# Kernel optimization log

Hardware: AMD Instinct MI355X
Metric: run time of the kernel (lower is better)

The kernel has to match this reference:

```python
import jax, jax.numpy as jnp
import numpy as np

N_NODES = 100000

def gcn_conv(x, W, b, src, dst, n):
    # PyG GCNConv with add_self_loops=True, symmetric normalization.
    # Transform first (reduces feature dim before irregular aggregation).
    h = x @ W  # [N, out]
    # degree with self loops: in-degree over dst plus 1 per node
    deg = jax.ops.segment_sum(jnp.ones_like(dst, dtype=h.dtype), dst, num_segments=n) + 1.0
    dinv = jax.lax.rsqrt(deg)  # deg >= 1 due to self loops
    norm = dinv[src] * dinv[dst]  # [E]
    # message = norm * h[src], aggregated at dst; self-loop term = dinv_i^2 * h_i
    agg = jax.ops.segment_sum(h[src] * norm[:, None], dst, num_segments=n)
    agg = agg + h * (dinv * dinv)[:, None]
    return agg + b

def setup_inputs() -> dict:
    key = jax.random.key(0)
    k1, k2, k3, k4, k5 = jax.random.split(key, 5)
    F_in, H, E_dim = 128, 64, 64
    node_features = jax.random.normal(k1, (N_NODES, F_in), dtype=jnp.float32)
    edge_index = jax.random.randint(k2, (2, 1600000), 0, N_NODES, dtype=jnp.int64)
    s = 1.0 / np.sqrt(F_in)
    W1 = jax.random.uniform(k3, (F_in, H), jnp.float32, -s, s)
    b1 = jnp.zeros((H,), jnp.float32)
    s2 = 1.0 / np.sqrt(H)
    W2 = jax.random.uniform(k4, (H, H), jnp.float32, -s2, s2)
    b2 = jnp.zeros((H,), jnp.float32)
    Wl = jax.random.uniform(k5, (H, E_dim), jnp.float32, -s2, s2)
    bl = jnp.zeros((E_dim,), jnp.float32)
    return {"node_features": node_features, "edge_index": edge_index,
            "W1": W1, "b1": b1, "W2": W2, "b2": b2, "Wl": Wl, "bl": bl}

def reference(node_features, edge_index, W1, b1, W2, b2, Wl, bl):
    src, dst = edge_index[0], edge_index[1]
    n = node_features.shape[0]
    x = node_features.astype(jnp.float32)
    x = jax.nn.relu(gcn_conv(x, W1, b1, src, dst, n))
    # dropout: train=False -> identity
    x = jax.nn.relu(gcn_conv(x, W2, b2, src, dst, n))
    x = x @ Wl + bl
    return jax.nn.sigmoid(x).T  # [embed_size, N]
```

## Files before the change

### kernel.cpp

```cpp
#include <hip/hip_runtime.h>
#include <hip/hip_bf16.h>


#define FEAT 64
#define FIN 128
#define PAD 64
#define CAP 4608
#define EPB 4096
#define MAXNB 512

typedef __attribute__((ext_vector_type(8))) short  short8;
typedef __attribute__((ext_vector_type(4))) float  f32x4;

__device__ __forceinline__ unsigned short f2bf(float f) {
    union { float f; unsigned u; } x; x.f = f;
    unsigned r = x.u + 0x7FFF + ((x.u >> 16) & 1);
    return (unsigned short)(r >> 16);
}
__device__ __forceinline__ float bflo(unsigned u) {
    union { unsigned v; float f; } x; x.v = u << 16; return x.f;
}
__device__ __forceinline__ float bfhi(unsigned u) {
    union { unsigned v; float f; } x; x.v = u & 0xFFFF0000u; return x.f;
}

__global__ void wtrans_kernel(const float* __restrict__ W1, const float* __restrict__ W2,
                              unsigned short* __restrict__ Wt1, unsigned short* __restrict__ Wt2) {
    int t = blockIdx.x * 256 + threadIdx.x;
    if (t < FIN * 64) {
        int k = t >> 6, n = t & 63;
        Wt1[n * FIN + k] = f2bf(W1[t]);
    } else if (t < FIN * 64 + 64 * 64) {
        int u = t - FIN * 64;
        int k = u >> 6, n = u & 63;
        Wt2[n * 64 + k] = f2bf(W2[u]);
    }
}

__global__ __launch_bounds__(256) void bin_kernel(const int* __restrict__ ei,
                                                  int* __restrict__ bcnt,
                                                  int* __restrict__ bbuf,
                                                  int E, int nb) {
    __shared__ int hist[MAXNB];
    __shared__ int base[MAXNB];
    __shared__ int cur[MAXNB];
    for (int t = threadIdx.x; t < nb; t += 256) { hist[t] = 0; cur[t] = 0; }
    __syncthreads();
    int e0 = blockIdx.x * EPB;
    int sreg[16], dreg[16];
#pragma unroll
    for (int k = 0; k < 16; ++k) {
        int idx = e0 + k * 256 + threadIdx.x;
        if (idx < E) {
            sreg[k] = ei[idx];
            dreg[k] = ei[E + idx];
            atomicAdd(&hist[dreg[k] >> 8], 1);
        } else {
            dreg[k] = -1;
        }
    }
    __syncthreads();
    for (int t = threadIdx.x; t < nb; t += 256) {
        int h = hist[t];
        base[t] = (h > 0) ? atomicAdd(&bcnt[t * 16], h) : 0;
    }
    __syncthreads();
#pragma unroll
    for (int k = 0; k < 16; ++k) {
        if (dreg[k] >= 0) {
            int b = dreg[k] >> 8;
            int p = base[b] + atomicAdd(&cur[b], 1);
            if (p < CAP)
                bbuf[(size_t)b * CAP + p] = sreg[k] | ((dreg[k] & 255) << 20);
        }
    }
}

__global__ __launch_bounds__(256) void ell_from_bins_kernel(const int* __restrict__ bbuf,
                                                            const int* __restrict__ bcnt,
                                                            int* __restrict__ col,
                                                            int* __restrict__ cnt,
                                                            float* __restrict__ dinv,
                                                            unsigned int* __restrict__ gz,
                                                            int N) {
    __shared__ int lcnt[256];
    int b = blockIdx.x;
    int d0 = b << 8;
    lcnt[threadIdx.x] = 0;
    if (b == 0 && threadIdx.x < 32)
        gz[(size_t)N * 32 + threadIdx.x] = 0u;
    __syncthreads();
    int ne = bcnt[b * 16];
    if (ne > CAP) ne = CAP;
    const int* eb = bbuf + (size_t)b * CAP;
    for (int i = threadIdx.x; i < ne; i += 256) {
        int w = eb[i];
        int s = w & 0xFFFFF;
        int dl = w >> 20;
        int slot = atomicAdd(&lcnt[dl], 1);
        if (slot < PAD) col[(size_t)(d0 + dl) * PAD + slot] = s;
    }
    __syncthreads();
    int d = d0 + threadIdx.x;
    if (d < N) {
        int c = lcnt[threadIdx.x];
        if (c > PAD) c = PAD;
        int c8 = (c + 7) & ~7;
        for (int k = c; k < c8; ++k) col[(size_t)d * PAD + k] = N;
        cnt[d] = c;
        dinv[d] = rsqrtf((float)c + 1.0f);
    }
}

template<int K>
__global__ __launch_bounds__(256) void gemm_mfma_kernel(const float* __restrict__ x,
                                                        const unsigned short* __restrict__ Wt,
                                                        const float* __restrict__ dinv,
                                                        unsigned short* __restrict__ g, int N) {
    const int lane = threadIdx.x & 63;
    const int wave = threadIdx.x >> 6;
    const int m = lane & 15, quad = lane >> 4;
    const int r0 = blockIdx.x * 64 + wave * 16;
    const int arow = r0 + m;
    const bool aok = arow < N;
    f32x4 acc[4] = {f32x4{0,0,0,0}, f32x4{0,0,0,0}, f32x4{0,0,0,0}, f32x4{0,0,0,0}};
    union { short8 s; unsigned short u[8]; } a;
#pragma unroll
    for (int s = 0; s < K / 32; ++s) {
        if (aok) {
            const float* xp = x + (size_t)arow * K + s * 32 + quad * 8;
            float4 a0 = *(const float4*)xp;
            float4 a1 = *(const float4*)(xp + 4);
            a.u[0] = f2bf(a0.x); a.u[1] = f2bf(a0.y);
            a.u[2] = f2bf(a0.z); a.u[3] = f2bf(a0.w);
            a.u[4] = f2bf(a1.x); a.u[5] = f2bf(a1.y);
            a.u[6] = f2bf(a1.z); a.u[7] = f2bf(a1.w);
        } else {
#pragma unroll
            for (int k = 0; k < 8; ++k) a.u[k] = 0;
        }
#pragma unroll
        for (int t = 0; t < 4; ++t) {
            const unsigned short* bp = Wt + (size_t)(t * 16 + m) * K + s * 32 + quad * 8;
            short8 bf = *(const short8*)bp;
            acc[t] = __builtin_amdgcn_mfma_f32_16x16x32_bf16(a.s, bf, acc[t], 0, 0, 0);
        }
    }
    const int rbase = r0 + quad * 4;
#pragma unroll
    for (int i = 0; i < 4; ++i) {
        int r = rbase + i;
        if (r < N) {
            float di = dinv[r];
#pragma unroll
            for (int t = 0; t < 4; ++t)
                g[(size_t)r * 64 + t * 16 + m] = f2bf(di * acc[t][i]);
        }
    }
}

__global__ __launch_bounds__(256) void agg_relu_kernel(const unsigned short* __restrict__ g,
                                                       const int* __restrict__ cnt,
                                                       const int* __restrict__ col,
                                                       const float* __restrict__ dinv,
                                                       const float* __restrict__ b,
                                                       float* __restrict__ xout, int N) {
    int node = blockIdx.x * 4 + (threadIdx.x >> 6);
    if (node >= N) return;
    int lane = threadIdx.x & 63;
    int rg = lane >> 3, fc = lane & 7;
    int c = cnt[node];
    if (c > PAD) c = PAD;
    int c8 = (c + 7) & ~7;
    const int* cl = col + (size_t)node * PAD;
    float acc[8] = {0.f, 0.f, 0.f, 0.f, 0.f, 0.f, 0.f, 0.f};
#pragma unroll 2
    for (int j = 0; j < c8; j += 8) {
        int s = cl[j + rg];
        uint4 w = *(const uint4*)(g + (size_t)s * 64 + fc * 8);
        acc[0] += bflo(w.x); acc[1] += bfhi(w.x);
        acc[2] += bflo(w.y); acc[3] += bfhi(w.y);
        acc[4] += bflo(w.z); acc[5] += bfhi(w.z);
        acc[6] += bflo(w.w); acc[7] += bfhi(w.w);
    }
#pragma unroll
    for (int mk = 8; mk <= 32; mk <<= 1)
#pragma unroll
        for (int k = 0; k < 8; ++k)
            acc[k] += __shfl_xor(acc[k], mk, 64);
    if (rg == 0) {
        uint4 w = *(const uint4*)(g + (size_t)node * 64 + fc * 8);
        acc[0] += bflo(w.x); acc[1] += bfhi(w.x);
        acc[2] += bflo(w.y); acc[3] += bfhi(w.y);
        acc[4] += bflo(w.z); acc[5] += bfhi(w.z);
        acc[6] += bflo(w.w); acc[7] += bfhi(w.w);
        float di = dinv[node];
        float4 b0 = *(const float4*)&b[fc * 8];
        float4 b1 = *(const float4*)&b[fc * 8 + 4];
        float4 o0 = make_float4(fmaxf(di * acc[0] + b0.x, 0.f),
                                fmaxf(di * acc[1] + b0.y, 0.f),
                                fmaxf(di * acc[2] + b0.z, 0.f),
                                fmaxf(di * acc[3] + b0.w, 0.f));
        float4 o1 = make_float4(fmaxf(di * acc[4] + b1.x, 0.f),
                                fmaxf(di * acc[5] + b1.y, 0.f),
                                fmaxf(di * acc[6] + b1.z, 0.f),
                                fmaxf(di * acc[7] + b1.w, 0.f));
        *(float4*)&xout[(size_t)node * 64 + fc * 8]     = o0;
        *(float4*)&xout[(size_t)node * 64 + fc * 8 + 4] = o1;
    }
}

__global__ __launch_bounds__(256) void final_kernel(const float* __restrict__ x2,
                                                    const float* __restrict__ Wl,
                                                    const float* __restrict__ bl,
                                                    float* __restrict__ out, int N) {
    __shared__ float xs[64 * 68];
    __shared__ float ws[64 * 64];
    __shared__ float bls[64];
    const int tid = threadIdx.x;
    const int r0 = blockIdx.x * 64;
    for (int t = tid * 4; t < 64 * 64; t += 1024)
        *(float4*)&ws[t] = *(const float4*)&Wl[t];
    if (tid < 64) bls[tid] = bl[tid];
    for (int t = tid; t < 64 * 16; t += 256) {
        int row = t >> 4, f = (t & 15) * 4;
        int r = r0 + row;
        float4 v = make_float4(0.f, 0.f, 0.f, 0.f);
        if (r < N) v = *(const float4*)&x2[(size_t)r * 64 + f];
        *(float4*)&xs[row * 68 + f] = v;
    }
    __syncthreads();
    const int ty = tid >> 4, tx = tid & 15;
    float acc[4][4] = {};
    float a[4][4], b[4][4];
#pragma unroll 2
    for (int kk = 0; kk < 64; kk += 4) {
#pragma unroll
        for (int dr = 0; dr < 4; ++dr)
            *(float4*)a[dr] = *(float4*)&xs[(4 * ty + dr) * 68 + kk];
#pragma unroll
        for (int dj = 0; dj < 4; ++dj)
            *(float4*)b[dj] = *(float4*)&ws[(kk + dj) * 64 + 4 * tx];
#pragma unroll
        for (int dj = 0; dj < 4; ++dj)
#pragma unroll
            for (int dr = 0; dr < 4; ++dr)
#pragma unroll
                for (int dc = 0; dc < 4; ++dc)
                    acc[dr][dc] = fmaf(a[dr][dj], b[dj][dc], acc[dr][dc]);
    }
    float4 bv = *(float4*)&bls[4 * tx];
    float bb[4] = { bv.x, bv.y, bv.z, bv.w };
    __syncthreads();
    float* ot = xs;
#pragma unroll
    for (int dr = 0; dr < 4; ++dr)
#pragma unroll
        for (int dc = 0; dc < 4; ++dc) {
            float v = acc[dr][dc] + bb[dc];
            ot[(4 * ty + dr) * 65 + 4 * tx + dc] = 1.f / (1.f + __expf(-v));
        }
    __syncthreads();
    int il = tid & 63, jg = tid >> 6;
    int i = r0 + il;
    if (i < N)
#pragma unroll
        for (int it = 0; it < 16; ++it) {
            int j = it * 4 + jg;
            out[(size_t)j * N + i] = ot[il * 65 + j];
        }
}

extern "C" void kernel_launch(void* const* d_in, const int* in_sizes, int n_in,
                              void* d_out, int out_size, void* d_ws, size_t ws_size,
                              hipStream_t stream) {
    const float* x   = (const float*)d_in[0];
    const int*   ei  = (const int*)d_in[1];
    const float* W1  = (const float*)d_in[2];
    const float* b1  = (const float*)d_in[3];
    const float* W2  = (const float*)d_in[4];
    const float* b2  = (const float*)d_in[5];
    const float* Wl  = (const float*)d_in[6];
    const float* bl  = (const float*)d_in[7];
    float*       out = (float*)d_out;

    int N  = in_sizes[0] / FIN;
    int E  = in_sizes[1] / 2;
    int nb = (N + 255) >> 8;
    int ng = (N + 63) >> 6;

    int*            bcnt = (int*)d_ws;
    unsigned short* Wt1  = (unsigned short*)(bcnt + MAXNB * 16);
    unsigned short* Wt2  = Wt1 + FIN * 64;
    int*            cnt  = (int*)(Wt2 + 64 * 64);
    float*          dinv = (float*)(cnt + N);
    int*            col  = (int*)(dinv + N);
    int*            bbuf = col + (size_t)N * PAD;
    unsigned short* bufG = (unsigned short*)bbuf;
    float*          bufX = (float*)(bufG + (size_t)(N + 1) * FEAT);

    wtrans_kernel<<<(FIN * 64 + 64 * 64 + 255) / 256, 256, 0, stream>>>(W1, W2, Wt1, Wt2);

    hipMemsetAsync(bcnt, 0, MAXNB * 16 * sizeof(int), stream);
    bin_kernel<<<(E + EPB - 1) / EPB, 256, 0, stream>>>(ei, bcnt, bbuf, E, nb);
    ell_from_bins_kernel<<<nb, 256, 0, stream>>>(bbuf, bcnt, col, cnt, dinv,
                                                 (unsigned int*)bufG, N);

    gemm_mfma_kernel<FIN><<<ng, 256, 0, stream>>>(x, Wt1, dinv, bufG, N);
    agg_relu_kernel<<<(N + 3) / 4, 256, 0, stream>>>(bufG, cnt, col, dinv, b1, bufX, N);

    gemm_mfma_kernel<FEAT><<<ng, 256, 0, stream>>>(bufX, Wt2, dinv, bufG, N);
    agg_relu_kernel<<<(N + 3) / 4, 256, 0, stream>>>(bufG, cnt, col, dinv, b2, bufX, N);

    final_kernel<<<ng, 256, 0, stream>>>(bufX, Wl, bl, out, N);
}
```

Measured before the change: 284.0 us.

## Store intermediate activations in bf16 and use MFMA for final linear layer

After: 275.4 us. 1.03x faster.

```diff
diff --git a/kernel.cpp b/kernel.cpp
--- a/kernel.cpp
+++ b/kernel.cpp
@@ -25,7 +25,9 @@
 }
 
 __global__ void wtrans_kernel(const float* __restrict__ W1, const float* __restrict__ W2,
-                              unsigned short* __restrict__ Wt1, unsigned short* __restrict__ Wt2) {
+                              const float* __restrict__ Wl,
+                              unsigned short* __restrict__ Wt1, unsigned short* __restrict__ Wt2,
+                              unsigned short* __restrict__ Wlt, int* __restrict__ bcnt) {
     int t = blockIdx.x * 256 + threadIdx.x;
     if (t < FIN * 64) {
         int k = t >> 6, n = t & 63;
@@ -34,6 +36,12 @@
         int u = t - FIN * 64;
         int k = u >> 6, n = u & 63;
         Wt2[n * 64 + k] = f2bf(W2[u]);
+    } else if (t < FIN * 64 + 2 * 64 * 64) {
+        int u = t - FIN * 64 - 64 * 64;
+        int k = u >> 6, n = u & 63;
+        Wlt[n * 64 + k] = f2bf(Wl[u]);
+    } else if (t < FIN * 64 + 2 * 64 * 64 + MAXNB * 16) {
+        bcnt[t - FIN * 64 - 2 * 64 * 64] = 0;
     }
 }
 
@@ -112,11 +120,10 @@
     }
 }
 
-template<int K>
-__global__ __launch_bounds__(256) void gemm_mfma_kernel(const float* __restrict__ x,
-                                                        const unsigned short* __restrict__ Wt,
-                                                        const float* __restrict__ dinv,
-                                                        unsigned short* __restrict__ g, int N) {
+__global__ __launch_bounds__(256) void gemm1_mfma_kernel(const float* __restrict__ x,
+                                                         const unsigned short* __restrict__ Wt,
+                                                         const float* __restrict__ dinv,
+                                                         unsigned short* __restrict__ g, int N) {
     const int lane = threadIdx.x & 63;
     const int wave = threadIdx.x >> 6;
     const int m = lane & 15, quad = lane >> 4;
@@ -126,9 +133,9 @@
     f32x4 acc[4] = {f32x4{0,0,0,0}, f32x4{0,0,0,0}, f32x4{0,0,0,0}, f32x4{0,0,0,0}};
     union { short8 s; unsigned short u[8]; } a;
 #pragma unroll
-    for (int s = 0; s < K / 32; ++s) {
+    for (int s = 0; s < FIN / 32; ++s) {
         if (aok) {
-            const float* xp = x + (size_t)arow * K + s * 32 + quad * 8;
+            const float* xp = x + (size_t)arow * FIN + s * 32 + quad * 8;
             float4 a0 = *(const float4*)xp;
             float4 a1 = *(const float4*)(xp + 4);
             a.u[0] = f2bf(a0.x); a.u[1] = f2bf(a0.y);
@@ -141,9 +148,43 @@
         }
 #pragma unroll
         for (int t = 0; t < 4; ++t) {
-            const unsigned short* bp = Wt + (size_t)(t * 16 + m) * K + s * 32 + quad * 8;
+            const unsigned short* bp = Wt + (size_t)(t * 16 + m) * FIN + s * 32 + quad * 8;
             short8 bf = *(const short8*)bp;
             acc[t] = __builtin_amdgcn_mfma_f32_16x16x32_bf16(a.s, bf, acc[t], 0, 0, 0);
+        }
+    }
+    const int rbase = r0 + quad * 4;
+#pragma unroll
+    for (int i = 0; i < 4; ++i) {
+        int r = rbase + i;
+        if (r < N) {
+            float di = dinv[r];
+#pragma unroll
+            for (int t = 0; t < 4; ++t)
+                g[(size_t)r * 64 + t * 16 + m] = f2bf(di * acc[t][i]);
+        }
+    }
+}
+
+__global__ __launch_bounds__(256) void gemm2_mfma_kernel(const unsigned short* __restrict__ xb,
+                                                         const unsigned short* __restrict__ Wt,
+                                                         const float* __restrict__ dinv,
+                                                         unsigned short* __restrict__ g, int N) {
+    const int lane = threadIdx.x & 63;
+    const int wave = threadIdx.x >> 6;
+    const int m = lane & 15, quad = lane >> 4;
+    const int r0 = blockIdx.x * 64 + wave * 16;
+    const int arow = r0 + m;
+    const bool aok = arow < N;
+    f32x4 acc[4] = {f32x4{0,0,0,0}, f32x4{0,0,0,0}, f32x4{0,0,0,0}, f32x4{0,0,0,0}};
+    const short8 zero8 = short8{0,0,0,0,0,0,0,0};
+#pragma unroll
+    for (int s = 0; s < 2; ++s) {
+        short8 a = aok ? *(const short8*)(xb + (size_t)arow * 64 + s * 32 + quad * 8) : zero8;
+#pragma unroll
+        for (int t = 0; t < 4; ++t) {
+            short8 bf = *(const short8*)(Wt + (size_t)(t * 16 + m) * 64 + s * 32 + quad * 8);
+            acc[t] = __builtin_amdgcn_mfma_f32_16x16x32_bf16(a, bf, acc[t], 0, 0, 0);
         }
     }
     const int rbase = r0 + quad * 4;
@@ -164,7 +205,7 @@
                                                        const int* __restrict__ col,
                                                        const float* __restrict__ dinv,
                                                        const float* __restrict__ b,
-                                                       float* __restrict__ xout, int N) {
+                                                       unsigned short* __restrict__ xout, int N) {
     int node = blockIdx.x * 4 + (threadIdx.x >> 6);
     if (node >= N) return;
     int lane = threadIdx.x & 63;
@@ -197,78 +238,66 @@
         float di = dinv[node];
         float4 b0 = *(const float4*)&b[fc * 8];
         float4 b1 = *(const float4*)&b[fc * 8 + 4];
-        float4 o0 = make_float4(fmaxf(di * acc[0] + b0.x, 0.f),
-                                fmaxf(di * acc[1] + b0.y, 0.f),
-                                fmaxf(di * acc[2] + b0.z, 0.f),
-                                fmaxf(di * acc[3] + b0.w, 0.f));
-        float4 o1 = make_float4(fmaxf(di * acc[4] + b1.x, 0.f),
-                                fmaxf(di * acc[5] + b1.y, 0.f),
-                                fmaxf(di * acc[6] + b1.z, 0.f),
-                                fmaxf(di * acc[7] + b1.w, 0.f));
-        *(float4*)&xout[(size_t)node * 64 + fc * 8]     = o0;
-        *(float4*)&xout[(size_t)node * 64 + fc * 8 + 4] = o1;
-    }
-}
-
-__global__ __launch_bounds__(256) void final_kernel(const float* __restrict__ x2,
-                                                    const float* __restrict__ Wl,
-                                                    const float* __restrict__ bl,
-                                                    float* __restrict__ out, int N) {
-    __shared__ float xs[64 * 68];
-    __shared__ float ws[64 * 64];
-    __shared__ float bls[64];
-    const int tid = threadIdx.x;
-    const int r0 = blockIdx.x * 64;
-    for (int t = tid * 4; t < 64 * 64; t += 1024)
-        *(float4*)&ws[t] = *(const float4*)&Wl[t];
-    if (tid < 64) bls[tid] = bl[tid];
-    for (int t = tid; t < 64 * 16; t += 256) {
-        int row = t >> 4, f = (t & 15) * 4;
-        int r = r0 + row;
-        float4 v = make_float4(0.f, 0.f, 0.f, 0.f);
-        if (r < N) v = *(const float4*)&x2[(size_t)r * 64 + f];
-        *(float4*)&xs[row * 68 + f] = v;
-    }
-    __syncthreads();
-    const int ty = tid >> 4, tx = tid & 15;
-    float acc[4][4] = {};
-    float a[4][4], b[4][4];
-#pragma unroll 2
-    for (int kk = 0; kk < 64; kk += 4) {
-#pragma unroll
-        for (int dr = 0; dr < 4; ++dr)
-            *(float4*)a[dr] = *(float4*)&xs[(4 * ty + dr) * 68 + kk];
-#pragma unroll
-        for (int dj = 0; dj < 4; ++dj)
-            *(float4*)b[dj] = *(float4*)&ws[(kk + dj) * 64 + 4 * tx];
-#pragma unroll
-        for (int dj = 0; dj < 4; ++dj)
-#pragma unroll
-            for (int dr = 0; dr < 4; ++dr)
-#pragma unroll
-                for (int dc = 0; dc < 4; ++dc)
-                    acc[dr][dc] = fmaf(a[dr][dj], b[dj][dc], acc[dr][dc]);
-    }
-    float4 bv = *(float4*)&bls[4 * tx];
-    float bb[4] = { bv.x, bv.y, bv.z, bv.w };
-    __syncthreads();
-    float* ot = xs;
-#pragma unroll
-    for (int dr = 0; dr < 4; ++dr)
-#pragma unroll
-        for (int dc = 0; dc < 4; ++dc) {
-            float v = acc[dr][dc] + bb[dc];
-            ot[(4 * ty + dr) * 65 + 4 * tx + dc] = 1.f / (1.f + __expf(-v));
-        }
-    __syncthreads();
-    int il = tid & 63, jg = tid >> 6;
-    int i = r0 + il;
-    if (i < N)
-#pragma unroll
-        for (int it = 0; it < 16; ++it) {
-            int j = it * 4 + jg;
-            out[(size_t)j * N + i] = ot[il * 65 + j];
-        }
+        union { uint4 v; unsigned short u[8]; } o;
+        o.u[0] = f2bf(fmaxf(di * acc[0] + b0.x, 0.f));
+        o.u[1] = f2bf(fmaxf(di * acc[1] + b0.y, 0.f));
+        o.u[2] = f2bf(fmaxf(di * acc[2] + b0.z, 0.f));
+        o.u[3] = f2bf(fmaxf(di * acc[3] + b0.w, 0.f));
+        o.u[4] = f2bf(fmaxf(di * acc[4] + b1.x, 0.f));
+        o.u[5] = f2bf(fmaxf(di * acc[5] + b1.y, 0.f));
+        o.u[6] = f2bf(fmaxf(di * acc[6] + b1.z, 0.f));
+        o.u[7] = f2bf(fmaxf(di * acc[7] + b1.w, 0.f));
+        *(uint4*)&xout[(size_t)node * 64 + fc * 8] = o.v;
+    }
+}
+
+__global__ __launch_bounds__(256) void final_mfma_kernel(const unsigned short* __restrict__ x2,
+                                                         const unsigned short* __restrict__ Wlt,
+                                                         const float* __restrict__ bl,
+                                                         float* __restrict__ out, int N) {
+    const int lane = threadIdx.x & 63;
+    const int wave = threadIdx.x >> 6;
+    const int m = lane & 15, quad = lane >> 4;
+    const int r0 = blockIdx.x * 64 + wave * 16;
+    const int arow = r0 + m;
+    const bool aok = arow < N;
+    f32x4 acc[4] = {f32x4{0,0,0,0}, f32x4{0,0,0,0}, f32x4{0,0,0,0}, f32x4{0,0,0,0}};
+    const short8 zero8 = short8{0,0,0,0,0,0,0,0};
+#pragma unroll
+    for (int s = 0; s < 2; ++s) {
+        short8 a = aok ? *(const short8*)(x2 + (size_t)arow * 64 + s * 32 + quad * 8) : zero8;
+#pragma unroll
+        for (int t = 0; t < 4; ++t) {
+            short8 bf = *(const short8*)(Wlt + (size_t)(t * 16 + m) * 64 + s * 32 + quad * 8);
+            acc[t] = __builtin_amdgcn_mfma_f32_16x16x32_bf16(a, bf, acc[t], 0, 0, 0);
+        }
+    }
+    const int rbase = r0 + quad * 4;
+    if (rbase + 3 < N && (N & 3) == 0) {
+#pragma unroll
+        for (int t = 0; t < 4; ++t) {
+            int j = t * 16 + m;
+            float bj = bl[j];
+            float4 o;
+            o.x = 1.f / (1.f + __expf(-(acc[t][0] + bj)));
+            o.y = 1.f / (1.f + __expf(-(acc[t][1] + bj)));
+            o.z = 1.f / (1.f + __expf(-(acc[t][2] + bj)));
+            o.w = 1.f / (1.f + __expf(-(acc[t][3] + bj)));
+            *(float4*)&out[(size_t)j * N + rbase] = o;
+        }
+    } else {
+#pragma unroll
+        for (int t = 0; t < 4; ++t) {
+            int j = t * 16 + m;
+            float bj = bl[j];
+#pragma unroll
+            for (int i = 0; i < 4; ++i) {
+                int r = rbase + i;
+                if (r < N)
+                    out[(size_t)j * N + r] = 1.f / (1.f + __expf(-(acc[t][i] + bj)));
+            }
+        }
+    }
 }
 
 extern "C" void kernel_launch(void* const* d_in, const int* in_sizes, int n_in,
@@ -292,25 +321,26 @@
     int*            bcnt = (int*)d_ws;
     unsigned short* Wt1  = (unsigned short*)(bcnt + MAXNB * 16);
     unsigned short* Wt2  = Wt1 + FIN * 64;
-    int*            cnt  = (int*)(Wt2 + 64 * 64);
+    unsigned short* Wlt  = Wt2 + 64 * 64;
+    int*            cnt  = (int*)(Wlt + 64 * 64);
     float*          dinv = (float*)(cnt + N);
     int*            col  = (int*)(dinv + N);
     int*            bbuf = col + (size_t)N * PAD;
     unsigned short* bufG = (unsigned short*)bbuf;
-    float*          bufX = (float*)(bufG + (size_t)(N + 1) * FEAT);
-
-    wtrans_kernel<<<(FIN * 64 + 64 * 64 + 255) / 256, 256, 0, stream>>>(W1, W2, Wt1, Wt2);
-
-    hipMemsetAsync(bcnt, 0, MAXNB * 16 * sizeof(int), stream);
+    unsigned short* bufX = bufG + (size_t)(N + 1) * FEAT;
+
+    int wtot = FIN * 64 + 2 * 64 * 64 + MAXNB * 16;
+    wtrans_kernel<<<(wtot + 255) / 256, 256, 0, stream>>>(W1, W2, Wl, Wt1, Wt2, Wlt, bcnt);
+
     bin_kernel<<<(E + EPB - 1) / EPB, 256, 0, stream>>>(ei, bcnt, bbuf, E, nb);
     ell_from_bins_kernel<<<nb, 256, 0, stream>>>(bbuf, bcnt, col, cnt, dinv,
                                                  (unsigned int*)bufG, N);
 
-    gemm_mfma_kernel<FIN><<<ng, 256, 0, stream>>>(x, Wt1, dinv, bufG, N);
+    gemm1_mfma_kernel<<<ng, 256, 0, stream>>>(x, Wt1, dinv, bufG, N);
     agg_relu_kernel<<<(N + 3) / 4, 256, 0, stream>>>(bufG, cnt, col, dinv, b1, bufX, N);
 
-    gemm_mfma_kernel<FEAT><<<ng, 256, 0, stream>>>(bufX, Wt2, dinv, bufG, N);
+    gemm2_mfma_kernel<<<ng, 256, 0, stream>>>(bufX, Wt2, dinv, bufG, N);
     agg_relu_kernel<<<(N + 3) / 4, 256, 0, stream>>>(bufG, cnt, col, dinv, b2, bufX, N);
 
-    final_kernel<<<ng, 256, 0, stream>>>(bufX, Wl, bl, out, N);
-}
+    final_mfma_kernel<<<ng, 256, 0, stream>>>(bufX, Wlt, bl, out, N);
+}
```
